# Optimization experiments

Measured on AMD Instinct MI355X. Metric: run time of the kernel, lower is better.

The kernel has to match this reference:

```python
import jax, jax.numpy as jnp
import numpy as np

N_TOTAL = 200000
DIM = 256
N_GRAPHS = 8192
N_ITERS = 6


def setup_inputs() -> dict:
    key = jax.random.key(0)
    k1, k2, k3, k4, k5, k6 = jax.random.split(key, 6)
    x = jax.random.normal(k1, (N_TOTAL, DIM), dtype=jnp.float32)
    batch = jnp.sort(jax.random.randint(k2, (N_TOTAL,), 0, N_GRAPHS)).astype(jnp.int32)
    bound = 1.0 / np.sqrt(DIM)
    W_ih = jax.random.uniform(k3, (4 * DIM, DIM), jnp.float32, -bound, bound)
    W_hh = jax.random.uniform(k4, (4 * DIM, DIM), jnp.float32, -bound, bound)
    b_ih = jax.random.uniform(k5, (4 * DIM,), jnp.float32, -bound, bound)
    b_hh = jax.random.uniform(k6, (4 * DIM,), jnp.float32, -bound, bound)
    return {"x": x, "batch": batch, "n_graphs": N_GRAPHS,
            "W_ih": W_ih, "W_hh": W_hh, "b_ih": b_ih, "b_hh": b_hh}


def _lstm_cell(inp, h, c, W_ih, W_hh, b_ih, b_hh):
    # PyTorch LSTMCell: gates ordered i, f, g, o
    gates = inp @ W_ih.T + b_ih + h @ W_hh.T + b_hh
    i, f, g, o = jnp.split(gates, 4, axis=-1)
    c_new = jax.nn.sigmoid(f) * c + jax.nn.sigmoid(i) * jnp.tanh(g)
    h_new = jax.nn.sigmoid(o) * jnp.tanh(c_new)
    return h_new, c_new


def reference(x, batch, n_graphs, W_ih, W_hh, b_ih, b_hh):
    dim = x.shape[1]
    h = jnp.zeros((n_graphs, dim), x.dtype)
    c = jnp.zeros((n_graphs, dim), x.dtype)
    readout = jnp.zeros((n_graphs, dim), x.dtype)
    for _ in range(N_ITERS):
        # attention scores per node: <x_v, q_{g(v)}>
        scores = jnp.sum(x * h[batch], axis=-1)  # (N,)
        # torch scatter_reduce_ amax with zero init includes the 0 -> max(seg_max, 0)
        seg_max = jax.ops.segment_max(scores, batch, num_segments=n_graphs,
                                      indices_are_sorted=True)
        seg_max = jnp.maximum(seg_max, 0.0)
        e = jnp.exp(scores - seg_max[batch])
        seg_sum = jax.ops.segment_sum(e, batch, num_segments=n_graphs,
                                      indices_are_sorted=True)
        w = e / (seg_sum[batch] + 1e-8)  # (N,)
        readout = jax.ops.segment_sum(x * w[:, None], batch, num_segments=n_graphs,
                                      indices_are_sorted=True)  # (G, dim)
        h, c = _lstm_cell(readout, h, c, W_ih, W_hh, b_ih, b_hh)
    return jnp.concatenate([h, readout], axis=-1)  # (G, 2*dim)
```

## Files before the change

### kernel.cpp

```cpp
#include <hip/hip_runtime.h>
#include <hip/hip_bf16.h>
#include <hip/hip_fp16.h>
#include <stdint.h>

#define DIM 256
#define NG 8192
#define KDIM 512
#define GDIM 1024
#define N_ITERS 6

#define BM 128
#define BN 128
#define BK 64

typedef __hip_bfloat16 bf16;
typedef __attribute__((ext_vector_type(8))) short bf16x8;
typedef __attribute__((ext_vector_type(4))) float f32x4;
typedef __attribute__((ext_vector_type(8))) unsigned short u16x8;
typedef __attribute__((ext_vector_type(4))) unsigned short u16x4;

__device__ __forceinline__ void async16(void* lds, const void* g) {
    __builtin_amdgcn_global_load_lds((const __attribute__((address_space(1))) void*)g,
                                     (__attribute__((address_space(3))) void*)lds, 16, 0, 0);
}
__device__ __forceinline__ float fast_sigmoid(float v) {
    return 1.0f / (1.0f + __expf(-v));
}
__device__ __forceinline__ float fast_tanh(float v) {
    float e = __expf(2.0f * v);
    return (e - 1.0f) / (e + 1.0f);
}
__device__ __forceinline__ unsigned short f2bf(float v) {
    __hip_bfloat16 t = __float2bfloat16(v);
    unsigned short u; __builtin_memcpy(&u, &t, 2); return u;
}
__device__ __forceinline__ unsigned short f2h(float v) {
    __half t = __float2half_rn(v);
    unsigned short u; __builtin_memcpy(&u, &t, 2); return u;
}
__device__ __forceinline__ float h2f(unsigned short u) {
    __half t; __builtin_memcpy(&t, &u, 2);
    return __half2float(t);
}

__global__ void k_prep(const int* __restrict__ batch, int n_nodes, int* __restrict__ offs,
                       const float* __restrict__ Wih, const float* __restrict__ Whh,
                       const float* __restrict__ bih, const float* __restrict__ bhh,
                       bf16* __restrict__ Wcat, float* __restrict__ bsum,
                       float* __restrict__ h, float* __restrict__ c, bf16* __restrict__ Acat0) {
    const int idx = blockIdx.x * blockDim.x + threadIdx.x;
    if (idx < NG * DIM) {
        h[idx] = 0.0f; c[idx] = 0.0f;
        Acat0[(size_t)(idx >> 8) * KDIM + DIM + (idx & 255)] = __float2bfloat16(0.0f);
    }
    if (idx < GDIM * KDIM) {
        const int n = idx >> 9;
        const int k = idx & (KDIM - 1);
        const int d = n >> 2, gate = n & 3;
        const int j = gate * DIM + d;
        const float v = (k < DIM) ? Wih[j * DIM + k] : Whh[j * DIM + (k - DIM)];
        Wcat[idx] = __float2bfloat16(v);
    }
    if (idx < GDIM) {
        const int d = idx >> 2, gate = idx & 3;
        const int j = gate * DIM + d;
        bsum[idx] = bih[j] + bhh[j];
    }
    if (idx < n_nodes) {
        const int b = batch[idx];
        const int bp = (idx == 0) ? -1 : batch[idx - 1];
        for (int g = bp + 1; g <= b; ++g) offs[g] = idx;
        if (idx == n_nodes - 1)
            for (int g = b + 1; g <= NG; ++g) offs[g] = n_nodes;
    }
}

template <bool FIRST, bool LAST>
__global__ __launch_bounds__(256) void k_att(const float* __restrict__ xf,
                                             unsigned short* __restrict__ xb,
                                             const float* __restrict__ h,
                                             const int* __restrict__ offs,
                                             float* __restrict__ rout,
                                             bf16* __restrict__ AcatOut) {
    const int wave = threadIdx.x >> 6;
    const int g = (blockIdx.x << 2) + wave;
    const int lane = threadIdx.x & 63;
    const int half = lane >> 5, hl = lane & 31;

    float hreg[8];
    {
        const float4 a = *(const float4*)&h[(size_t)g * DIM + hl * 8];
        const float4 b = *(const float4*)&h[(size_t)g * DIM + hl * 8 + 4];
        hreg[0] = a.x; hreg[1] = a.y; hreg[2] = a.z; hreg[3] = a.w;
        hreg[4] = b.x; hreg[5] = b.y; hreg[6] = b.z; hreg[7] = b.w;
    }

    const int start = offs[g], end = offs[g + 1];
    float racc[8] = {0, 0, 0, 0, 0, 0, 0, 0};
    float m = 0.0f;
    float s = 0.0f;

    for (int r0 = start; r0 < end; r0 += 2) {
        const int r = r0 + half;
        const bool valid = (r < end);
        float xv[8];
        float dt = 0.0f;
        if (valid) {
            if (FIRST) {
                const float4 a = *(const float4*)&xf[(size_t)r * DIM + hl * 8];
                const float4 b = *(const float4*)&xf[(size_t)r * DIM + hl * 8 + 4];
                xv[0] = a.x; xv[1] = a.y; xv[2] = a.z; xv[3] = a.w;
                xv[4] = b.x; xv[5] = b.y; xv[6] = b.z; xv[7] = b.w;
                u16x8 pk;
                #pragma unroll
                for (int j = 0; j < 8; ++j) pk[j] = f2h(xv[j]);
                *(u16x8*)&xb[(size_t)r * DIM + hl * 8] = pk;
            } else {
                const u16x8 pk = *(const u16x8*)&xb[(size_t)r * DIM + hl * 8];
                #pragma unroll
                for (int j = 0; j < 8; ++j) xv[j] = h2f(pk[j]);
            }
            #pragma unroll
            for (int j = 0; j < 8; ++j) dt = fmaf(xv[j], hreg[j], dt);
        }
        #pragma unroll
        for (int off = 16; off > 0; off >>= 1) dt += __shfl_xor(dt, off);
        if (valid) {
            const float mn = fmaxf(m, dt);
            const float al = __expf(m - mn);
            const float e  = __expf(dt - mn);
            s = s * al + e;
            #pragma unroll
            for (int j = 0; j < 8; ++j) racc[j] = fmaf(racc[j], al, e * xv[j]);
            m = mn;
        }
    }

    const float mo = __shfl_xor(m, 32);
    const float M  = fmaxf(m, mo);
    const float al = __expf(m - M);
    s *= al;
    #pragma unroll
    for (int j = 0; j < 8; ++j) racc[j] *= al;
    s += __shfl_xor(s, 32);
    #pragma unroll
    for (int j = 0; j < 8; ++j) racc[j] += __shfl_xor(racc[j], 32);
    const float inv = 1.0f / (s + 1e-8f);
    float o[8];
    #pragma unroll
    for (int j = 0; j < 8; ++j) o[j] = racc[j] * inv;

    if (half == 0) {
        u16x8 pk;
        #pragma unroll
        for (int j = 0; j < 8; ++j) pk[j] = f2bf(o[j]);
        *(u16x8*)&AcatOut[(size_t)g * KDIM + hl * 8] = pk;
    } else if (LAST) {
        *(float4*)&rout[(size_t)g * KDIM + hl * 8]     = make_float4(o[0], o[1], o[2], o[3]);
        *(float4*)&rout[(size_t)g * KDIM + hl * 8 + 4] = make_float4(o[4], o[5], o[6], o[7]);
    }
}

template <bool LAST>
__global__ __launch_bounds__(256) void k_gemm_cell(const bf16* __restrict__ A,
                                                   const bf16* __restrict__ W,
                                                   const float* __restrict__ bsum,
                                                   float* __restrict__ cst,
                                                   float* __restrict__ hst,
                                                   bf16* __restrict__ AcatN,
                                                   float* __restrict__ hout) {
    __shared__ union {
        struct { bf16 As[BM * BK]; bf16 Bs[BN * BK]; } st;
        float ep[32][132];
    } sm;

    const int tid = threadIdx.x;
    const int wave = tid >> 6, lane = tid & 63;
    const int m0 = blockIdx.x * BM;
    const int n0 = blockIdx.y * BN;
    const int wr = wave >> 1, wc = wave & 1;

    f32x4 acc[4][4] = {};
    const int chunk = lane & 7;

    for (int k0 = 0; k0 < KDIM; k0 += BK) {
        #pragma unroll
        for (int i = 0; i < 4; ++i) {
            const int grp = wave * 32 + i * 8;
            async16(&sm.st.As[grp * BK],
                    A + (size_t)(m0 + grp + (lane >> 3)) * KDIM + k0 + chunk * 8);
        }
        #pragma unroll
        for (int i = 0; i < 4; ++i) {
            const int grp = wave * 32 + i * 8;
            async16(&sm.st.Bs[grp * BK],
                    W + (size_t)(n0 + grp + (lane >> 3)) * KDIM + k0 + chunk * 8);
        }
        asm volatile("s_waitcnt vmcnt(0)" ::: "memory");
        __syncthreads();

        #pragma unroll
        for (int ks = 0; ks < BK; ks += 32) {
            bf16x8 a[4], b[4];
            #pragma unroll
            for (int mi = 0; mi < 4; ++mi)
                a[mi] = *(const bf16x8*)&sm.st.As[(wr * 64 + mi * 16 + (lane & 15)) * BK + ks + (lane >> 4) * 8];
            #pragma unroll
            for (int ni = 0; ni < 4; ++ni)
                b[ni] = *(const bf16x8*)&sm.st.Bs[(wc * 64 + ni * 16 + (lane & 15)) * BK + ks + (lane >> 4) * 8];
            #pragma unroll
            for (int mi = 0; mi < 4; ++mi)
                #pragma unroll
                for (int ni = 0; ni < 4; ++ni)
                    acc[mi][ni] = __builtin_amdgcn_mfma_f32_16x16x32_bf16(a[mi], b[ni], acc[mi][ni], 0, 0, 0);
        }
        __syncthreads();
    }

    float bv[4];
    #pragma unroll
    for (int ni = 0; ni < 4; ++ni)
        bv[ni] = bsum[n0 + wc * 64 + ni * 16 + (lane & 15)];

    const int d0 = n0 >> 2;
    const int lr = tid >> 3;
    const int dd = (tid & 7) * 4;

    #pragma unroll
    for (int mi = 0; mi < 4; ++mi) {
        __syncthreads();
        #pragma unroll
        for (int ni = 0; ni < 4; ++ni) {
            const int colL = wc * 64 + ni * 16 + (lane & 15);
            #pragma unroll
            for (int r = 0; r < 4; ++r) {
                const int lrow = wr * 16 + (lane >> 4) * 4 + r;
                sm.ep[lrow][colL] = acc[mi][ni][r] + bv[ni];
            }
        }
        __syncthreads();
        const int grow = m0 + (lr >> 4) * 64 + mi * 16 + (lr & 15);
        const int d = d0 + dd;
        float co[4], cn[4], hn[4];
        *(float4*)co = *(const float4*)&cst[(size_t)grow * DIM + d];
        u16x4 hb;
        #pragma unroll
        for (int j = 0; j < 4; ++j) {
            const float4 q = *(const float4*)&sm.ep[lr][(dd + j) * 4];
            cn[j] = fast_sigmoid(q.y) * co[j] + fast_sigmoid(q.x) * fast_tanh(q.z);
            hn[j] = fast_sigmoid(q.w) * fast_tanh(cn[j]);
            hb[j] = f2bf(hn[j]);
        }
        if (LAST) {
            *(float4*)&hout[(size_t)grow * KDIM + d] = *(float4*)hn;
        } else {
            *(float4*)&cst[(size_t)grow * DIM + d] = *(float4*)cn;
            *(float4*)&hst[(size_t)grow * DIM + d] = *(float4*)hn;
            *(u16x4*)&AcatN[(size_t)grow * KDIM + DIM + d] = hb;
        }
    }
}

extern "C" void kernel_launch(void* const* d_in, const int* in_sizes, int n_in,
                              void* d_out, int out_size, void* d_ws, size_t ws_size,
                              hipStream_t stream) {
    const float* x     = (const float*)d_in[0];
    const int*   batch = (const int*)d_in[1];
    const float* Wih   = (const float*)d_in[3];
    const float* Whh   = (const float*)d_in[4];
    const float* bih   = (const float*)d_in[5];
    const float* bhh   = (const float*)d_in[6];
    const int n_nodes  = in_sizes[0] / DIM;
    float* out = (float*)d_out;

    char* ws = (char*)d_ws;
    size_t off = 0;
    auto alloc = [&](size_t bytes) -> void* {
        off = (off + 255) & ~(size_t)255;
        void* p = ws + off;
        off += bytes;
        return p;
    };
    int*   offs  = (int*)  alloc((size_t)(NG + 1) * sizeof(int));
    bf16*  Wcat  = (bf16*) alloc((size_t)GDIM * KDIM * sizeof(bf16));
    float* bsum  = (float*)alloc((size_t)GDIM * sizeof(float));
    bf16*  Acat0 = (bf16*) alloc((size_t)NG * KDIM * sizeof(bf16));
    bf16*  Acat1 = (bf16*) alloc((size_t)NG * KDIM * sizeof(bf16));
    float* h     = (float*)alloc((size_t)NG * DIM * sizeof(float));
    float* c     = (float*)alloc((size_t)NG * DIM * sizeof(float));
    unsigned short* xb = (unsigned short*)alloc((size_t)n_nodes * DIM * sizeof(unsigned short));
    (void)ws_size; (void)n_in; (void)out_size;

    k_prep<<<NG * DIM / 256, 256, 0, stream>>>(batch, n_nodes, offs, Wih, Whh, bih, bhh,
                                               Wcat, bsum, h, c, Acat0);

    for (int it = 0; it < N_ITERS; ++it) {
        bf16* Ain  = (it & 1) ? Acat1 : Acat0;
        bf16* Aout = (it & 1) ? Acat0 : Acat1;
        if (it == 0)
            k_att<true, false><<<NG / 4, 256, 0, stream>>>(x, xb, h, offs, nullptr, Ain);
        else if (it < N_ITERS - 1)
            k_att<false, false><<<NG / 4, 256, 0, stream>>>(x, xb, h, offs, nullptr, Ain);
        else
            k_att<false, true><<<NG / 4, 256, 0, stream>>>(x, xb, h, offs, out + DIM, Ain);

        if (it < N_ITERS - 1)
            k_gemm_cell<false><<<dim3(NG / BM, GDIM / BN), 256, 0, stream>>>(
                Ain, Wcat, bsum, c, h, Aout, nullptr);
        else
            k_gemm_cell<true><<<dim3(NG / BM, GDIM / BN), 256, 0, stream>>>(
                Ain, Wcat, bsum, c, nullptr, nullptr, out);
    }
}
```

Measured before the change: 832.3 us.

## Fuse all LSTM iterations into one persistent kernel with LDS-resident state

Replaces the per-iteration attention and GEMM+cell kernel pairs with a single kernel where each 512-thread block owns 32 graphs for all six iterations. h, c and the concatenated bf16 A operand stay in LDS or registers, and weights are pre-shuffled into MFMA fragment order so they can be read straight from global or L2 without LDS staging. The attention loop also prefetches the next row. This removes twelve launches and the global round-trips of h, c and Acat. In exchange, each block recomputes a 32x1024x512 GEMM that streams the full 1 MB weight matrix from cache per iteration, and only 256 blocks run, which may limit occupancy and load balance.

Measured after the change: 1.036 ms. 24.5% more time.

```diff
diff --git a/kernel.cpp b/kernel.cpp
--- a/kernel.cpp
+++ b/kernel.cpp
@@ -8,21 +8,15 @@
 #define KDIM 512
 #define GDIM 1024
 #define N_ITERS 6
-
-#define BM 128
-#define BN 128
-#define BK 64
+#define GPB 32
+#define NBLK (NG / GPB)
+#define NTHR 512
 
 typedef __hip_bfloat16 bf16;
 typedef __attribute__((ext_vector_type(8))) short bf16x8;
 typedef __attribute__((ext_vector_type(4))) float f32x4;
 typedef __attribute__((ext_vector_type(8))) unsigned short u16x8;
-typedef __attribute__((ext_vector_type(4))) unsigned short u16x4;
-
-__device__ __forceinline__ void async16(void* lds, const void* g) {
-    __builtin_amdgcn_global_load_lds((const __attribute__((address_space(1))) void*)g,
-                                     (__attribute__((address_space(3))) void*)lds, 16, 0, 0);
-}
+
 __device__ __forceinline__ float fast_sigmoid(float v) {
     return 1.0f / (1.0f + __expf(-v));
 }
@@ -43,31 +37,44 @@
     return __half2float(t);
 }
 
-__global__ void k_prep(const int* __restrict__ batch, int n_nodes, int* __restrict__ offs,
-                       const float* __restrict__ Wih, const float* __restrict__ Whh,
-                       const float* __restrict__ bih, const float* __restrict__ bhh,
-                       bf16* __restrict__ Wcat, float* __restrict__ bsum,
-                       float* __restrict__ h, float* __restrict__ c, bf16* __restrict__ Acat0) {
+struct SM {
+    unsigned short Acat[GPB * KDIM];
+    float h[GPB * DIM];
+};
+
+__global__ __launch_bounds__(256) void k_prep(const int* __restrict__ batch, int n_nodes,
+        int* __restrict__ offs,
+        const float* __restrict__ Wih, const float* __restrict__ Whh,
+        const float* __restrict__ bih, const float* __restrict__ bhh,
+        bf16* __restrict__ Wfrag, float* __restrict__ bsum) {
     const int idx = blockIdx.x * blockDim.x + threadIdx.x;
-    if (idx < NG * DIM) {
-        h[idx] = 0.0f; c[idx] = 0.0f;
-        Acat0[(size_t)(idx >> 8) * KDIM + DIM + (idx & 255)] = __float2bfloat16(0.0f);
-    }
-    if (idx < GDIM * KDIM) {
-        const int n = idx >> 9;
-        const int k = idx & (KDIM - 1);
-        const int d = n >> 2, gate = n & 3;
-        const int j = gate * DIM + d;
-        const float v = (k < DIM) ? Wih[j * DIM + k] : Whh[j * DIM + (k - DIM)];
-        Wcat[idx] = __float2bfloat16(v);
+    if (idx < 64 * 16 * 64) {
+        const int nfrag = idx >> 10;
+        const int kstep = (idx >> 6) & 15;
+        const int lane  = idx & 63;
+        const int c  = nfrag * 16 + (lane & 15);
+        const int k0 = kstep * 32 + (lane >> 4) * 8;
+        const int d  = ((c >> 7) << 5) | (c & 31);
+        const int gt = (c >> 5) & 3;
+        const int jsrc = gt * DIM + d;
+        u16x8 pk;
+        #pragma unroll
+        for (int j = 0; j < 8; ++j) {
+            const int k = k0 + j;
+            const float v = (k < DIM) ? Wih[(size_t)jsrc * DIM + k]
+                                      : Whh[(size_t)jsrc * DIM + (k - DIM)];
+            pk[j] = f2bf(v);
+        }
+        *(u16x8*)&Wfrag[(size_t)idx * 8] = pk;
     }
     if (idx < GDIM) {
-        const int d = idx >> 2, gate = idx & 3;
-        const int j = gate * DIM + d;
-        bsum[idx] = bih[j] + bhh[j];
+        const int d  = ((idx >> 7) << 5) | (idx & 31);
+        const int gt = (idx >> 5) & 3;
+        const int jsrc = gt * DIM + d;
+        bsum[idx] = bih[jsrc] + bhh[jsrc];
     }
     if (idx < n_nodes) {
-        const int b = batch[idx];
+        const int b  = batch[idx];
         const int bp = (idx == 0) ? -1 : batch[idx - 1];
         for (int g = bp + 1; g <= b; ++g) offs[g] = idx;
         if (idx == n_nodes - 1)
@@ -76,56 +83,67 @@
 }
 
 template <bool FIRST, bool LAST>
-__global__ __launch_bounds__(256) void k_att(const float* __restrict__ xf,
-                                             unsigned short* __restrict__ xb,
-                                             const float* __restrict__ h,
-                                             const int* __restrict__ offs,
-                                             float* __restrict__ rout,
-                                             bf16* __restrict__ AcatOut) {
-    const int wave = threadIdx.x >> 6;
-    const int g = (blockIdx.x << 2) + wave;
-    const int lane = threadIdx.x & 63;
+__device__ __forceinline__ void att_phase(int w, int lane, int g0,
+        const float* __restrict__ xf, unsigned short* __restrict__ xb,
+        const int* __restrict__ offs, float* __restrict__ out,
+        SM& sm, int nmax) {
     const int half = lane >> 5, hl = lane & 31;
-
-    float hreg[8];
-    {
-        const float4 a = *(const float4*)&h[(size_t)g * DIM + hl * 8];
-        const float4 b = *(const float4*)&h[(size_t)g * DIM + hl * 8 + 4];
-        hreg[0] = a.x; hreg[1] = a.y; hreg[2] = a.z; hreg[3] = a.w;
-        hreg[4] = b.x; hreg[5] = b.y; hreg[6] = b.z; hreg[7] = b.w;
-    }
-
-    const int start = offs[g], end = offs[g + 1];
-    float racc[8] = {0, 0, 0, 0, 0, 0, 0, 0};
-    float m = 0.0f;
-    float s = 0.0f;
-
-    for (int r0 = start; r0 < end; r0 += 2) {
-        const int r = r0 + half;
-        const bool valid = (r < end);
-        float xv[8];
-        float dt = 0.0f;
-        if (valid) {
-            if (FIRST) {
-                const float4 a = *(const float4*)&xf[(size_t)r * DIM + hl * 8];
-                const float4 b = *(const float4*)&xf[(size_t)r * DIM + hl * 8 + 4];
-                xv[0] = a.x; xv[1] = a.y; xv[2] = a.z; xv[3] = a.w;
-                xv[4] = b.x; xv[5] = b.y; xv[6] = b.z; xv[7] = b.w;
-                u16x8 pk;
-                #pragma unroll
-                for (int j = 0; j < 8; ++j) pk[j] = f2h(xv[j]);
-                *(u16x8*)&xb[(size_t)r * DIM + hl * 8] = pk;
+    for (int gi = 0; gi < 4; ++gi) {
+        const int gl = (w << 2) + gi;
+        const int g  = g0 + gl;
+        float hreg[8];
+        {
+            const float4 a = *(const float4*)&sm.h[gl * DIM + hl * 8];
+            const float4 b = *(const float4*)&sm.h[gl * DIM + hl * 8 + 4];
+            hreg[0] = a.x; hreg[1] = a.y; hreg[2] = a.z; hreg[3] = a.w;
+            hreg[4] = b.x; hreg[5] = b.y; hreg[6] = b.z; hreg[7] = b.w;
+        }
+        const int start = offs[g], end = offs[g + 1];
+        float m = 0.0f;
+        float s = 0.0f;
+        float racc[8] = {0, 0, 0, 0, 0, 0, 0, 0};
+        int r = start + half;
+
+        float pf[8];
+        u16x8 pk;
+        {
+            const size_t ap = (size_t)min(r, nmax) * DIM + hl * 8;
+            if constexpr (FIRST) {
+                const float4 a = *(const float4*)&xf[ap];
+                const float4 b = *(const float4*)&xf[ap + 4];
+                pf[0] = a.x; pf[1] = a.y; pf[2] = a.z; pf[3] = a.w;
+                pf[4] = b.x; pf[5] = b.y; pf[6] = b.z; pf[7] = b.w;
             } else {
-                const u16x8 pk = *(const u16x8*)&xb[(size_t)r * DIM + hl * 8];
+                pk = *(const u16x8*)&xb[ap];
+            }
+        }
+        for (; r < end; r += 2) {
+            float xv[8];
+            if constexpr (FIRST) {
+                #pragma unroll
+                for (int j = 0; j < 8; ++j) xv[j] = pf[j];
+            } else {
                 #pragma unroll
                 for (int j = 0; j < 8; ++j) xv[j] = h2f(pk[j]);
             }
+            const size_t ap = (size_t)min(r + 2, nmax) * DIM + hl * 8;
+            if constexpr (FIRST) {
+                const float4 a = *(const float4*)&xf[ap];
+                const float4 b = *(const float4*)&xf[ap + 4];
+                pf[0] = a.x; pf[1] = a.y; pf[2] = a.z; pf[3] = a.w;
+                pf[4] = b.x; pf[5] = b.y; pf[6] = b.z; pf[7] = b.w;
+                u16x8 st;
+                #pragma unroll
+                for (int j = 0; j < 8; ++j) st[j] = f2h(xv[j]);
+                *(u16x8*)&xb[(size_t)r * DIM + hl * 8] = st;
+            } else {
+                pk = *(const u16x8*)&xb[ap];
+            }
+            float dt = 0.0f;
             #pragma unroll
             for (int j = 0; j < 8; ++j) dt = fmaf(xv[j], hreg[j], dt);
-        }
-        #pragma unroll
-        for (int off = 16; off > 0; off >>= 1) dt += __shfl_xor(dt, off);
-        if (valid) {
+            #pragma unroll
+            for (int off = 16; off > 0; off >>= 1) dt += __shfl_xor(dt, off);
             const float mn = fmaxf(m, dt);
             const float al = __expf(m - mn);
             const float e  = __expf(dt - mn);
@@ -134,130 +152,109 @@
             for (int j = 0; j < 8; ++j) racc[j] = fmaf(racc[j], al, e * xv[j]);
             m = mn;
         }
-    }
-
-    const float mo = __shfl_xor(m, 32);
-    const float M  = fmaxf(m, mo);
-    const float al = __expf(m - M);
-    s *= al;
+        const float mo = __shfl_xor(m, 32);
+        const float M  = fmaxf(m, mo);
+        const float am = __expf(m - M);
+        s *= am;
+        #pragma unroll
+        for (int j = 0; j < 8; ++j) racc[j] *= am;
+        s += __shfl_xor(s, 32);
+        #pragma unroll
+        for (int j = 0; j < 8; ++j) racc[j] += __shfl_xor(racc[j], 32);
+        const float inv = 1.0f / (s + 1e-8f);
+        if (half == 0) {
+            u16x8 ob;
+            #pragma unroll
+            for (int j = 0; j < 8; ++j) ob[j] = f2bf(racc[j] * inv);
+            unsigned off = (unsigned)(gl * 1024 + hl * 16);
+            off ^= (unsigned)((gl & 7) << 4);
+            *(u16x8*)((char*)sm.Acat + off) = ob;
+        } else if (LAST) {
+            float o[8];
+            #pragma unroll
+            for (int j = 0; j < 8; ++j) o[j] = racc[j] * inv;
+            *(float4*)&out[(size_t)g * KDIM + DIM + hl * 8]     = make_float4(o[0], o[1], o[2], o[3]);
+            *(float4*)&out[(size_t)g * KDIM + DIM + hl * 8 + 4] = make_float4(o[4], o[5], o[6], o[7]);
+        }
+    }
+}
+
+__global__ __launch_bounds__(NTHR) void k_fused(const float* __restrict__ xf,
+        unsigned short* __restrict__ xb, const int* __restrict__ offs,
+        const bf16* __restrict__ Wfrag, const float* __restrict__ bsum,
+        float* __restrict__ out, int n_nodes) {
+    __shared__ SM sm;
+    const int tid  = threadIdx.x;
+    const int w    = tid >> 6, lane = tid & 63;
+    const int g0   = blockIdx.x * GPB;
+    const int nmax = n_nodes - 1;
+
+    for (int i = tid; i < GPB * KDIM; i += NTHR) sm.Acat[i] = 0;
+    for (int i = tid; i < GPB * DIM;  i += NTHR) sm.h[i] = 0.0f;
+
+    float c_[2][2][4] = {};
+    float bv[8];
     #pragma unroll
-    for (int j = 0; j < 8; ++j) racc[j] *= al;
-    s += __shfl_xor(s, 32);
-    #pragma unroll
-    for (int j = 0; j < 8; ++j) racc[j] += __shfl_xor(racc[j], 32);
-    const float inv = 1.0f / (s + 1e-8f);
-    float o[8];
-    #pragma unroll
-    for (int j = 0; j < 8; ++j) o[j] = racc[j] * inv;
-
-    if (half == 0) {
-        u16x8 pk;
-        #pragma unroll
-        for (int j = 0; j < 8; ++j) pk[j] = f2bf(o[j]);
-        *(u16x8*)&AcatOut[(size_t)g * KDIM + hl * 8] = pk;
-    } else if (LAST) {
-        *(float4*)&rout[(size_t)g * KDIM + hl * 8]     = make_float4(o[0], o[1], o[2], o[3]);
-        *(float4*)&rout[(size_t)g * KDIM + hl * 8 + 4] = make_float4(o[4], o[5], o[6], o[7]);
-    }
-}
-
-template <bool LAST>
-__global__ __launch_bounds__(256) void k_gemm_cell(const bf16* __restrict__ A,
-                                                   const bf16* __restrict__ W,
-                                                   const float* __restrict__ bsum,
-                                                   float* __restrict__ cst,
-                                                   float* __restrict__ hst,
-                                                   bf16* __restrict__ AcatN,
-                                                   float* __restrict__ hout) {
-    __shared__ union {
-        struct { bf16 As[BM * BK]; bf16 Bs[BN * BK]; } st;
-        float ep[32][132];
-    } sm;
-
-    const int tid = threadIdx.x;
-    const int wave = tid >> 6, lane = tid & 63;
-    const int m0 = blockIdx.x * BM;
-    const int n0 = blockIdx.y * BN;
-    const int wr = wave >> 1, wc = wave & 1;
-
-    f32x4 acc[4][4] = {};
-    const int chunk = lane & 7;
-
-    for (int k0 = 0; k0 < KDIM; k0 += BK) {
-        #pragma unroll
-        for (int i = 0; i < 4; ++i) {
-            const int grp = wave * 32 + i * 8;
-            async16(&sm.st.As[grp * BK],
-                    A + (size_t)(m0 + grp + (lane >> 3)) * KDIM + k0 + chunk * 8);
-        }
-        #pragma unroll
-        for (int i = 0; i < 4; ++i) {
-            const int grp = wave * 32 + i * 8;
-            async16(&sm.st.Bs[grp * BK],
-                    W + (size_t)(n0 + grp + (lane >> 3)) * KDIM + k0 + chunk * 8);
-        }
-        asm volatile("s_waitcnt vmcnt(0)" ::: "memory");
+    for (int nf = 0; nf < 8; ++nf) bv[nf] = bsum[w * 128 + nf * 16 + (lane & 15)];
+
+    __syncthreads();
+
+    const bf16* wb = Wfrag + (size_t)w * 65536 + (size_t)lane * 8;
+
+    for (int it = 0; it < N_ITERS; ++it) {
+        if (it == 0)                att_phase<true,  false>(w, lane, g0, xf, xb, offs, out, sm, nmax);
+        else if (it < N_ITERS - 1)  att_phase<false, false>(w, lane, g0, xf, xb, offs, out, sm, nmax);
+        else                        att_phase<false, true >(w, lane, g0, xf, xb, offs, out, sm, nmax);
         __syncthreads();
 
-        #pragma unroll
-        for (int ks = 0; ks < BK; ks += 32) {
-            bf16x8 a[4], b[4];
-            #pragma unroll
-            for (int mi = 0; mi < 4; ++mi)
-                a[mi] = *(const bf16x8*)&sm.st.As[(wr * 64 + mi * 16 + (lane & 15)) * BK + ks + (lane >> 4) * 8];
-            #pragma unroll
-            for (int ni = 0; ni < 4; ++ni)
-                b[ni] = *(const bf16x8*)&sm.st.Bs[(wc * 64 + ni * 16 + (lane & 15)) * BK + ks + (lane >> 4) * 8];
-            #pragma unroll
-            for (int mi = 0; mi < 4; ++mi)
-                #pragma unroll
-                for (int ni = 0; ni < 4; ++ni)
-                    acc[mi][ni] = __builtin_amdgcn_mfma_f32_16x16x32_bf16(a[mi], b[ni], acc[mi][ni], 0, 0, 0);
+        f32x4 acc[2][8] = {};
+        #pragma unroll
+        for (int kstep = 0; kstep < 16; ++kstep) {
+            const int r0 = lane & 15;
+            unsigned o0 = (unsigned)(r0 * 1024 + kstep * 64 + (lane >> 4) * 16)
+                        ^ (unsigned)((r0 & 7) << 4);
+            unsigned o1 = o0 + 16 * 1024;
+            const bf16x8 a0 = *(const bf16x8*)((const char*)sm.Acat + o0);
+            const bf16x8 a1 = *(const bf16x8*)((const char*)sm.Acat + o1);
+            #pragma unroll
+            for (int nf = 0; nf < 8; ++nf) {
+                const bf16x8 b = *(const bf16x8*)&wb[(size_t)nf * 8192 + kstep * 512];
+                acc[0][nf] = __builtin_amdgcn_mfma_f32_16x16x32_bf16(a0, b, acc[0][nf], 0, 0, 0);
+                acc[1][nf] = __builtin_amdgcn_mfma_f32_16x16x32_bf16(a1, b, acc[1][nf], 0, 0, 0);
+            }
         }
         __syncthreads();
-    }
-
-    float bv[4];
-    #pragma unroll
-    for (int ni = 0; ni < 4; ++ni)
-        bv[ni] = bsum[n0 + wc * 64 + ni * 16 + (lane & 15)];
-
-    const int d0 = n0 >> 2;
-    const int lr = tid >> 3;
-    const int dd = (tid & 7) * 4;
-
-    #pragma unroll
-    for (int mi = 0; mi < 4; ++mi) {
+
+        #pragma unroll
+        for (int mf = 0; mf < 2; ++mf) {
+            #pragma unroll
+            for (int dhi = 0; dhi < 2; ++dhi) {
+                const int d = w * 32 + dhi * 16 + (lane & 15);
+                #pragma unroll
+                for (int rr = 0; rr < 4; ++rr) {
+                    const int row = mf * 16 + (lane >> 4) * 4 + rr;
+                    const float gi = acc[mf][0 + dhi][rr] + bv[0 + dhi];
+                    const float gf = acc[mf][2 + dhi][rr] + bv[2 + dhi];
+                    const float gg = acc[mf][4 + dhi][rr] + bv[4 + dhi];
+                    const float go = acc[mf][6 + dhi][rr] + bv[6 + dhi];
+                    const float cn = fast_sigmoid(gf) * c_[mf][dhi][rr]
+                                   + fast_sigmoid(gi) * fast_tanh(gg);
+                    const float hn = fast_sigmoid(go) * fast_tanh(cn);
+                    c_[mf][dhi][rr] = cn;
+                    sm.h[row * DIM + d] = hn;
+                    unsigned ho = (unsigned)(row * 1024 + (DIM + d) * 2)
+                                ^ (unsigned)((row & 7) << 4);
+                    *(unsigned short*)((char*)sm.Acat + ho) = f2bf(hn);
+                }
+            }
+        }
         __syncthreads();
-        #pragma unroll
-        for (int ni = 0; ni < 4; ++ni) {
-            const int colL = wc * 64 + ni * 16 + (lane & 15);
-            #pragma unroll
-            for (int r = 0; r < 4; ++r) {
-                const int lrow = wr * 16 + (lane >> 4) * 4 + r;
-                sm.ep[lrow][colL] = acc[mi][ni][r] + bv[ni];
-            }
-        }
-        __syncthreads();
-        const int grow = m0 + (lr >> 4) * 64 + mi * 16 + (lr & 15);
-        const int d = d0 + dd;
-        float co[4], cn[4], hn[4];
-        *(float4*)co = *(const float4*)&cst[(size_t)grow * DIM + d];
-        u16x4 hb;
-        #pragma unroll
-        for (int j = 0; j < 4; ++j) {
-            const float4 q = *(const float4*)&sm.ep[lr][(dd + j) * 4];
-            cn[j] = fast_sigmoid(q.y) * co[j] + fast_sigmoid(q.x) * fast_tanh(q.z);
-            hn[j] = fast_sigmoid(q.w) * fast_tanh(cn[j]);
-            hb[j] = f2bf(hn[j]);
-        }
-        if (LAST) {
-            *(float4*)&hout[(size_t)grow * KDIM + d] = *(float4*)hn;
-        } else {
-            *(float4*)&cst[(size_t)grow * DIM + d] = *(float4*)cn;
-            *(float4*)&hst[(size_t)grow * DIM + d] = *(float4*)hn;
-            *(u16x4*)&AcatN[(size_t)grow * KDIM + DIM + d] = hb;
-        }
+    }
+
+    for (int i = tid; i < GPB * 64; i += NTHR) {
+        const int row = i >> 6;
+        const int dq  = (i & 63) << 2;
+        *(float4*)&out[(size_t)(g0 + row) * KDIM + dq] = *(const float4*)&sm.h[row * DIM + dq];
     }
 }
 
@@ -282,33 +279,14 @@
         return p;
     };
     int*   offs  = (int*)  alloc((size_t)(NG + 1) * sizeof(int));
-    bf16*  Wcat  = (bf16*) alloc((size_t)GDIM * KDIM * sizeof(bf16));
+    bf16*  Wfrag = (bf16*) alloc((size_t)GDIM * KDIM * sizeof(bf16));
     float* bsum  = (float*)alloc((size_t)GDIM * sizeof(float));
-    bf16*  Acat0 = (bf16*) alloc((size_t)NG * KDIM * sizeof(bf16));
-    bf16*  Acat1 = (bf16*) alloc((size_t)NG * KDIM * sizeof(bf16));
-    float* h     = (float*)alloc((size_t)NG * DIM * sizeof(float));
-    float* c     = (float*)alloc((size_t)NG * DIM * sizeof(float));
     unsigned short* xb = (unsigned short*)alloc((size_t)n_nodes * DIM * sizeof(unsigned short));
     (void)ws_size; (void)n_in; (void)out_size;
 
-    k_prep<<<NG * DIM / 256, 256, 0, stream>>>(batch, n_nodes, offs, Wih, Whh, bih, bhh,
-                                               Wcat, bsum, h, c, Acat0);
-
-    for (int it = 0; it < N_ITERS; ++it) {
-        bf16* Ain  = (it & 1) ? Acat1 : Acat0;
-        bf16* Aout = (it & 1) ? Acat0 : Acat1;
-        if (it == 0)
-            k_att<true, false><<<NG / 4, 256, 0, stream>>>(x, xb, h, offs, nullptr, Ain);
-        else if (it < N_ITERS - 1)
-            k_att<false, false><<<NG / 4, 256, 0, stream>>>(x, xb, h, offs, nullptr, Ain);
-        else
-            k_att<false, true><<<NG / 4, 256, 0, stream>>>(x, xb, h, offs, out + DIM, Ain);
-
-        if (it < N_ITERS - 1)
-            k_gemm_cell<false><<<dim3(NG / BM, GDIM / BN), 256, 0, stream>>>(
-                Ain, Wcat, bsum, c, h, Aout, nullptr);
-        else
-            k_gemm_cell<true><<<dim3(NG / BM, GDIM / BN), 256, 0, stream>>>(
-                Ain, Wcat, bsum, c, nullptr, nullptr, out);
-    }
-}
+    const int cover = (n_nodes > 64 * 16 * 64) ? n_nodes : 64 * 16 * 64;
+    const int pb = (cover + 255) / 256;
+
+    k_prep<<<pb, 256, 0, stream>>>(batch, n_nodes, offs, Wih, Whh, bih, bhh, Wfrag, bsum);
+    k_fused<<<NBLK, NTHR, 0, stream>>>(x, xb, offs, Wfrag, bsum, out, n_nodes);
+}
```
